# Optimization experiments

Hardware: AMD Instinct MI355X
Metric: run time of the kernel (lower is better)

Reference implementation:

```python
import jax, jax.numpy as jnp
import numpy as np

B, T, C, HS = 4, 2048, 1024, 128

def setup_inputs() -> dict:
    key = jax.random.key(0)
    k0, k1, k2, k3 = jax.random.split(key, 4)
    scale = 1.0 / np.sqrt(C)
    return {
        "x": jax.random.normal(k0, (B, T, C), dtype=jnp.float32),
        "Wk": jax.random.normal(k1, (C, HS), dtype=jnp.float32) * scale,
        "Wq": jax.random.normal(k2, (C, HS), dtype=jnp.float32) * scale,
        "Wv": jax.random.normal(k3, (C, HS), dtype=jnp.float32) * scale,
    }

def reference(x, Wk, Wq, Wv):
    # k, q, v: [B, T, HS]
    k = jnp.einsum('btc,ch->bth', x, Wk)
    q = jnp.einsum('btc,ch->bth', x, Wq)
    v = jnp.einsum('btc,ch->bth', x, Wv)
    hs = k.shape[-1]
    # full T x T scores (no causal mask in source), scaled by head_size**-0.5
    wei = jnp.einsum('bqh,bkh->bqk', q, k) * (hs ** -0.5)
    wei = jax.nn.softmax(wei, axis=-1)
    # dropout p=0.0 -> identity
    out = jnp.einsum('bqk,bkh->bqh', wei, v)
    return out
```

## Files before the change

kernel.cpp:

```cpp
#include <hip/hip_runtime.h>
#include <hip/hip_bf16.h>

typedef float  f32x4 __attribute__((ext_vector_type(4)));
typedef float  f32x8 __attribute__((ext_vector_type(8)));
typedef short  s8v   __attribute__((ext_vector_type(8)));
typedef __bf16 b8v   __attribute__((ext_vector_type(8)));
typedef unsigned int u32;
typedef unsigned short ushort;

#define T_DIM  2048
#define C_DIM  1024


typedef const __attribute__((address_space(1))) u32 gu32;
typedef __attribute__((address_space(3))) u32 lu32;

static __device__ __forceinline__ void glds16(const void* g, void* l) {
  __builtin_amdgcn_global_load_lds((gu32*)g, (lu32*)l, 16, 0, 0);
}

static __device__ __forceinline__ b8v ldb8(const ushort* p) {
  return __builtin_bit_cast(b8v, *reinterpret_cast<const s8v*>(p));
}

static __device__ __forceinline__ b8v cvt8(f32x8 v) {
  b8v r;
#pragma unroll
  for (int i = 0; i < 8; ++i) r[i] = (__bf16)v[i];
  return r;
}

static __device__ __forceinline__ ushort bfu(float f) {
  __bf16 h = (__bf16)f;
  return __builtin_bit_cast(ushort, h);
}

static __device__ __forceinline__ f32x4 mfma16(b8v a, b8v b, f32x4 c) {
  return __builtin_amdgcn_mfma_f32_16x16x32_bf16(a, b, c, 0, 0, 0);
}

#define BAR_VM(N)                                                        \
  asm volatile("s_waitcnt vmcnt(" #N ") lgkmcnt(0)" ::: "memory");       \
  __builtin_amdgcn_s_barrier();                                          \
  asm volatile("" ::: "memory");

#define BAR_PLAIN                                                        \
  asm volatile("" ::: "memory");                                         \
  __builtin_amdgcn_s_barrier();                                          \
  asm volatile("" ::: "memory");

__global__ __launch_bounds__(256) void wconv(const float* __restrict__ Wq,
                                             const float* __restrict__ Wk,
                                             const float* __restrict__ Wv,
                                             ushort* __restrict__ Wt) {
  __shared__ float lds[64][65];
  const int m  = blockIdx.z;
  const int c0 = blockIdx.x * 64;
  const int h0 = blockIdx.y * 64;
  const float* W = (m == 0) ? Wq : (m == 1) ? Wk : Wv;

  const int cl = threadIdx.x >> 4;
  const int h4 = (threadIdx.x & 15) * 4;
#pragma unroll
  for (int i = 0; i < 4; ++i) {
    int c = cl + i * 16;
    float4 v = *reinterpret_cast<const float4*>(W + (c0 + c) * 128 + h0 + h4);
    lds[c][h4] = v.x; lds[c][h4 + 1] = v.y;
    lds[c][h4 + 2] = v.z; lds[c][h4 + 3] = v.w;
  }
  __syncthreads();
  const int hl = threadIdx.x >> 2;
  const int cs = (threadIdx.x & 3) * 16;
  s8v o0, o1;
#pragma unroll
  for (int i = 0; i < 8; ++i) o0[i] = (short)bfu(lds[cs + i][hl]);
#pragma unroll
  for (int i = 0; i < 8; ++i) o1[i] = (short)bfu(lds[cs + 8 + i][hl]);
  ushort* dst = Wt + (m * 128 + h0 + hl) * C_DIM + c0 + cs;
  *reinterpret_cast<s8v*>(dst) = o0;
  *reinterpret_cast<s8v*>(dst + 8) = o1;
}

__global__ __launch_bounds__(256) void proj(const float* __restrict__ x,
                                            const ushort* __restrict__ Wt,
                                            ushort* __restrict__ q,
                                            ushort* __restrict__ k,
                                            ushort* __restrict__ vt) {
  __shared__ __align__(16) ushort Ab[2][32 * 72];
  __shared__ __align__(16) ushort Bb[2][128 * 64];
  __shared__ __align__(16) ushort stage[5120];

  const int t   = threadIdx.x;
  const int w   = t >> 6;
  const int lid = t & 63;
  const int lr  = lid & 15;
  const int g   = lid >> 4;
  const int wr  = w >> 1;
  const int wc  = w & 1;
  const int m   = blockIdx.y;
  const int r0  = blockIdx.x * 32;

  const int arow = t >> 3;
  const int acol = (t & 7) * 8;
  const float* ag = x + (r0 + arow) * C_DIM + acol;

  const int bswz = (((lid & 7) ^ (lid >> 3)) << 4);
  const char* bg = (const char*)(Wt + m * 128 * C_DIM);

  f32x4 acc[4] = {};

#pragma unroll
  for (int j = 0; j < 4; ++j) {
    int h = j * 32 + w * 8 + (lid >> 3);
    glds16(bg + h * 2048 + bswz, (char*)&Bb[0][0] + j * 4096 + w * 1024);
  }
  {
    f32x8 av = *reinterpret_cast<const f32x8*>(ag);
    b8v ac = cvt8(av);
    *reinterpret_cast<s8v*>(&Ab[0][arow * 72 + acol]) =
        __builtin_bit_cast(s8v, ac);
  }
  __syncthreads();

  int cur = 0;
#pragma unroll 1
  for (int i = 0; i < 16; ++i) {
    const int nxt = cur ^ 1;
    f32x8 an;
    if (i < 15) {
      const int kk = (i + 1) * 64;
#pragma unroll
      for (int j = 0; j < 4; ++j) {
        int h = j * 32 + w * 8 + (lid >> 3);
        glds16(bg + h * 2048 + kk * 2 + bswz,
               (char*)&Bb[nxt][0] + j * 4096 + w * 1024);
      }
      an = *reinterpret_cast<const f32x8*>(ag + kk);
    }

#pragma unroll
    for (int kk2 = 0; kk2 < 2; ++kk2) {
      b8v af = ldb8(&Ab[cur][(wr * 16 + lr) * 72 + kk2 * 32 + g * 8]);
#pragma unroll
      for (int cn = 0; cn < 4; ++cn) {
        int h = wc * 64 + cn * 16 + lr;
        int inner = (kk2 * 64 + g * 16) ^ ((h & 7) << 4);
        b8v bf = ldb8(
            (const ushort*)((const char*)&Bb[cur][h * 64] + inner));
        acc[cn] = mfma16(af, bf, acc[cn]);
      }
    }

    if (i < 15) {
      b8v anc = cvt8(an);
      *reinterpret_cast<s8v*>(&Ab[nxt][arow * 72 + acol]) =
          __builtin_bit_cast(s8v, anc);
    }
    __syncthreads();
    cur = nxt;
  }

  if (m < 2) {
#pragma unroll
    for (int cn = 0; cn < 4; ++cn)
#pragma unroll
      for (int j = 0; j < 4; ++j)
        stage[(wr * 16 + 4 * g + j) * 136 + wc * 64 + cn * 16 + lr] =
            bfu(acc[cn][j]);
    __syncthreads();
    ushort* dst = (m == 0) ? q : k;
#pragma unroll
    for (int c = 0; c < 2; ++c) {
      int chunk = c * 256 + t;
      int row = chunk >> 4, col8 = chunk & 15;
      s8v v8 = *reinterpret_cast<const s8v*>(&stage[row * 136 + col8 * 8]);
      *reinterpret_cast<s8v*>(&dst[(r0 + row) * 128 + col8 * 8]) = v8;
    }
  } else {
#pragma unroll
    for (int cn = 0; cn < 4; ++cn)
#pragma unroll
      for (int j = 0; j < 4; ++j)
        stage[(wc * 64 + cn * 16 + lr) * 40 + wr * 16 + 4 * g + j] =
            bfu(acc[cn][j]);
    __syncthreads();
    int b = blockIdx.x >> 6;
    int tbase = (blockIdx.x & 63) * 32;
#pragma unroll
    for (int c = 0; c < 2; ++c) {
      int chunk = c * 256 + t;
      int h = chunk >> 2, t8 = chunk & 3;
      s8v v8 = *reinterpret_cast<const s8v*>(&stage[h * 40 + t8 * 8]);
      *reinterpret_cast<s8v*>(&vt[(b * 128 + h) * T_DIM + tbase + t8 * 8]) = v8;
    }
  }
}

__global__ __launch_bounds__(256) void attn(const ushort* __restrict__ q,
                                            const ushort* __restrict__ k,
                                            const ushort* __restrict__ vt,
                                            float* __restrict__ out) {
  extern __shared__ __align__(16) char smem[];

  const int t   = threadIdx.x;
  const int w   = t >> 6;
  const int lid = t & 63;
  const int lr  = lid & 15;
  const int g   = lid >> 4;
  const int wh  = w >> 1;
  const int wk  = w & 1;
  const int b   = blockIdx.y;
  const int t0  = blockIdx.x * 16;

  const ushort* qp = q + (b * T_DIM + t0) * 128;
  b8v aq[4];
#pragma unroll
  for (int kf = 0; kf < 4; ++kf)
    aq[kf] = ldb8(&qp[lr * 128 + kf * 32 + g * 8]);

  const char* kgb = (const char*)(k + b * T_DIM * 128);
  const char* vgb = (const char*)(vt + b * 128 * T_DIM);
  const char* ksrc[4];
  const char* vsrc[4];
#pragma unroll
  for (int j = 0; j < 4; ++j) {
    ksrc[j] = kgb + (16 * w + 4 * j + (lid >> 4)) * 256 +
              (((lid & 15) ^ (4 * j + (lid >> 4))) << 4);
    vsrc[j] = vgb + ((w * 4 + j) * 8 + (lid >> 3)) * 4096 +
              (((lid & 7) ^ (lid >> 3)) << 4);
  }

  const int rbase = wk * 32 + 8 * (lr >> 2) + (lr & 3);
  int koff[2][4], voff[4];
#pragma unroll
  for (int tt = 0; tt < 2; ++tt)
#pragma unroll
    for (int kf = 0; kf < 4; ++kf)
      koff[tt][kf] = (rbase + 4 * tt) * 256 +
                     (((kf * 4 + g) ^ ((rbase + 4 * tt) & 15)) << 4);
#pragma unroll
  for (int hf = 0; hf < 4; ++hf)
    voff[hf] = 16384 + (wh * 64 + hf * 16 + lr) * 128 +
               (((wk * 4 + g) ^ (lr & 7)) << 4);

  f32x4 of[4] = {};
  float lsum = 0.0f;
  const float scale = 0.08838834764831845f;

#define ATTN_STAGE(KV0, BUF)                                              \
  _Pragma("unroll") for (int j = 0; j < 4; ++j)                           \
      glds16(ksrc[j] + (KV0) * 256,                                       \
             smem + (BUF) * 32768 + (w * 4 + j) * 1024);                  \
  _Pragma("unroll") for (int j = 0; j < 4; ++j)                           \
      glds16(vsrc[j] + (KV0) * 2,                                         \
             smem + (BUF) * 32768 + 16384 + (w * 4 + j) * 1024);

#define ATTN_BODY(BUF)                                                    \
  {                                                                       \
    const char* Kb = smem + (BUF) * 32768;                                \
    b8v kf0[4], kf1[4], vf[4];                                            \
    _Pragma("unroll") for (int kf = 0; kf < 4; ++kf)                      \
        kf0[kf] = ldb8((const ushort*)(Kb + koff[0][kf]));                \
    _Pragma("unroll") for (int kf = 0; kf < 4; ++kf)                      \
        kf1[kf] = ldb8((const ushort*)(Kb + koff[1][kf]));                \
    _Pragma("unroll") for (int hf = 0; hf < 4; ++hf)                      \
        vf[hf] = ldb8((const ushort*)(Kb + voff[hf]));                    \
    f32x4 s0 = {}, s1 = {};                                               \
    __builtin_amdgcn_s_setprio(1);                                        \
    _Pragma("unroll") for (int kf = 0; kf < 4; ++kf) {                    \
      s0 = mfma16(kf0[kf], aq[kf], s0);                                   \
      s1 = mfma16(kf1[kf], aq[kf], s1);                                   \
    }                                                                     \
    __builtin_amdgcn_s_setprio(0);                                        \
    b8v pk;                                                               \
    {                                                                     \
      float p0 = __expf(s0[0] * scale - 4.0f);                            \
      float p1 = __expf(s0[1] * scale - 4.0f);                            \
      float p2 = __expf(s0[2] * scale - 4.0f);                            \
      float p3 = __expf(s0[3] * scale - 4.0f);                            \
      float p4 = __expf(s1[0] * scale - 4.0f);                            \
      float p5 = __expf(s1[1] * scale - 4.0f);                            \
      float p6 = __expf(s1[2] * scale - 4.0f);                            \
      float p7 = __expf(s1[3] * scale - 4.0f);                            \
      lsum += ((p0 + p1) + (p2 + p3)) + ((p4 + p5) + (p6 + p7));          \
      pk[0] = (__bf16)p0; pk[1] = (__bf16)p1;                             \
      pk[2] = (__bf16)p2; pk[3] = (__bf16)p3;                             \
      pk[4] = (__bf16)p4; pk[5] = (__bf16)p5;                             \
      pk[6] = (__bf16)p6; pk[7] = (__bf16)p7;                             \
    }                                                                     \
    __builtin_amdgcn_s_setprio(1);                                        \
    _Pragma("unroll") for (int hf = 0; hf < 4; ++hf)                      \
        of[hf] = mfma16(pk, vf[hf], of[hf]);                              \
    __builtin_amdgcn_s_setprio(0);                                        \
  }

  ATTN_STAGE(0, 0)
  ATTN_STAGE(64, 1)

#pragma unroll 1
  for (int i = 0; i < 31; ++i) {
    BAR_VM(8)
    ATTN_BODY(i & 1)
    BAR_PLAIN
    if (i < 30) { ATTN_STAGE((i + 2) * 64, i & 1) }
  }
  BAR_VM(0)
  ATTN_BODY(1)

#undef ATTN_STAGE
#undef ATTN_BODY

  {
    float r = lsum;
    r += __shfl_xor(r, 16);
    r += __shfl_xor(r, 32);
    lsum = r;
  }

  float* lb = (float*)smem;
  float* ob = (float*)(smem + 256);
  __syncthreads();
  if (wh == 0 && g == 0) lb[wk * 16 + lr] = lsum;
  if (wk == 1) {
#pragma unroll
    for (int hf = 0; hf < 4; ++hf)
#pragma unroll
      for (int j = 0; j < 4; ++j)
        ob[(wh * 16 + 4 * g + j) * 64 + hf * 16 + lr] = of[hf][j];
  }
  __syncthreads();
  if (wk == 0) {
    float inv[4];
#pragma unroll
    for (int j = 0; j < 4; ++j)
      inv[j] = 1.0f / (lb[4 * g + j] + lb[16 + 4 * g + j]);
#pragma unroll
    for (int hf = 0; hf < 4; ++hf)
#pragma unroll
      for (int j = 0; j < 4; ++j) {
        int qrow = 4 * g + j;
        float val = of[hf][j] + ob[(wh * 16 + qrow) * 64 + hf * 16 + lr];
        out[(b * T_DIM + t0 + qrow) * 128 + wh * 64 + hf * 16 + lr] =
            val * inv[j];
      }
  }
}

extern "C" void kernel_launch(void* const* d_in, const int* in_sizes, int n_in,
                              void* d_out, int out_size, void* d_ws,
                              size_t ws_size, hipStream_t stream) {
  const float* x  = (const float*)d_in[0];
  const float* Wk = (const float*)d_in[1];
  const float* Wq = (const float*)d_in[2];
  const float* Wv = (const float*)d_in[3];
  float* out = (float*)d_out;

  char* ws = (char*)d_ws;
  ushort* Wt  = (ushort*)ws;
  ushort* qb  = (ushort*)(ws + (1u << 20));
  ushort* kb  = (ushort*)(ws + 3u * (1u << 20));
  ushort* vtb = (ushort*)(ws + 5u * (1u << 20));

  (void)hipFuncSetAttribute(reinterpret_cast<const void*>(&attn),
                            hipFuncAttributeMaxDynamicSharedMemorySize, 65536);

  wconv<<<dim3(16, 2, 3), dim3(256), 0, stream>>>(Wq, Wk, Wv, Wt);
  proj<<<dim3(256, 3), dim3(256), 0, stream>>>(x, Wt, qb, kb, vtb);
  attn<<<dim3(128, 4), dim3(256), 65536, stream>>>(qb, kb, vtb, out);
}
```

Measured before the change: 56.54 us.

## Use 8-wave attention blocks sharing K/V tiles with a triple-buffered single-barrier pipeline

The attention kernel now runs 512 threads per block covering 32 query rows, two groups of four waves, so each staged K/V tile in LDS serves twice as many queries and per-thread global-to-LDS loads are halved. The double-buffered loop with two barriers per iteration becomes a three-buffer ring with one barrier per iteration, issuing the next stage before computing the current one. This cuts redundant K/V fetches and barrier stalls but uses 96KB of LDS per block and halves the grid, which may reduce occupancy.

Result: faster. 51.62 us (-8.7%).

```diff
diff --git a/kernel.cpp b/kernel.cpp
--- a/kernel.cpp
+++ b/kernel.cpp
@@ -41,11 +41,6 @@
 
 #define BAR_VM(N)                                                        \
   asm volatile("s_waitcnt vmcnt(" #N ") lgkmcnt(0)" ::: "memory");       \
-  __builtin_amdgcn_s_barrier();                                          \
-  asm volatile("" ::: "memory");
-
-#define BAR_PLAIN                                                        \
-  asm volatile("" ::: "memory");                                         \
   __builtin_amdgcn_s_barrier();                                          \
   asm volatile("" ::: "memory");
 
@@ -196,7 +191,7 @@
   }
 }
 
-__global__ __launch_bounds__(256) void attn(const ushort* __restrict__ q,
+__global__ __launch_bounds__(512) void attn(const ushort* __restrict__ q,
                                             const ushort* __restrict__ k,
                                             const ushort* __restrict__ vt,
                                             float* __restrict__ out) {
@@ -207,12 +202,13 @@
   const int lid = t & 63;
   const int lr  = lid & 15;
   const int g   = lid >> 4;
-  const int wh  = w >> 1;
+  const int wq  = w >> 2;
+  const int wh  = (w >> 1) & 1;
   const int wk  = w & 1;
   const int b   = blockIdx.y;
-  const int t0  = blockIdx.x * 16;
-
-  const ushort* qp = q + (b * T_DIM + t0) * 128;
+  const int t0  = blockIdx.x * 32;
+
+  const ushort* qp = q + (b * T_DIM + t0 + wq * 16) * 128;
   b8v aq[4];
 #pragma unroll
   for (int kf = 0; kf < 4; ++kf)
@@ -220,13 +216,13 @@
 
   const char* kgb = (const char*)(k + b * T_DIM * 128);
   const char* vgb = (const char*)(vt + b * 128 * T_DIM);
-  const char* ksrc[4];
-  const char* vsrc[4];
-#pragma unroll
-  for (int j = 0; j < 4; ++j) {
-    ksrc[j] = kgb + (16 * w + 4 * j + (lid >> 4)) * 256 +
-              (((lid & 15) ^ (4 * j + (lid >> 4))) << 4);
-    vsrc[j] = vgb + ((w * 4 + j) * 8 + (lid >> 3)) * 4096 +
+  const char* ksrc[2];
+  const char* vsrc[2];
+#pragma unroll
+  for (int j = 0; j < 2; ++j) {
+    int krow = 8 * w + 4 * j + (lid >> 4);
+    ksrc[j] = kgb + krow * 256 + (((lid & 15) ^ (krow & 15)) << 4);
+    vsrc[j] = vgb + ((w * 2 + j) * 8 + (lid >> 3)) * 4096 +
               (((lid & 7) ^ (lid >> 3)) << 4);
   }
 
@@ -248,12 +244,12 @@
   const float scale = 0.08838834764831845f;
 
 #define ATTN_STAGE(KV0, BUF)                                              \
-  _Pragma("unroll") for (int j = 0; j < 4; ++j)                           \
+  _Pragma("unroll") for (int j = 0; j < 2; ++j)                           \
       glds16(ksrc[j] + (KV0) * 256,                                       \
-             smem + (BUF) * 32768 + (w * 4 + j) * 1024);                  \
-  _Pragma("unroll") for (int j = 0; j < 4; ++j)                           \
+             smem + (BUF) * 32768 + (w * 2 + j) * 1024);                  \
+  _Pragma("unroll") for (int j = 0; j < 2; ++j)                           \
       glds16(vsrc[j] + (KV0) * 2,                                         \
-             smem + (BUF) * 32768 + 16384 + (w * 4 + j) * 1024);
+             smem + (BUF) * 32768 + 16384 + (w * 2 + j) * 1024);
 
 #define ATTN_BODY(BUF)                                                    \
   {                                                                       \
@@ -297,15 +293,19 @@
   ATTN_STAGE(0, 0)
   ATTN_STAGE(64, 1)
 
+  int cur = 0;
 #pragma unroll 1
   for (int i = 0; i < 31; ++i) {
-    BAR_VM(8)
-    ATTN_BODY(i & 1)
-    BAR_PLAIN
-    if (i < 30) { ATTN_STAGE((i + 2) * 64, i & 1) }
+    BAR_VM(4)
+    if (i < 30) {
+      int nb = cur + 2; if (nb >= 3) nb -= 3;
+      ATTN_STAGE((i + 2) * 64, nb)
+    }
+    ATTN_BODY(cur)
+    ++cur; if (cur == 3) cur = 0;
   }
   BAR_VM(0)
-  ATTN_BODY(1)
+  ATTN_BODY(cur)
 
 #undef ATTN_STAGE
 #undef ATTN_BODY
@@ -320,27 +320,29 @@
   float* lb = (float*)smem;
   float* ob = (float*)(smem + 256);
   __syncthreads();
-  if (wh == 0 && g == 0) lb[wk * 16 + lr] = lsum;
+  if (wh == 0 && g == 0) lb[(wk * 2 + wq) * 16 + lr] = lsum;
   if (wk == 1) {
 #pragma unroll
     for (int hf = 0; hf < 4; ++hf)
 #pragma unroll
       for (int j = 0; j < 4; ++j)
-        ob[(wh * 16 + 4 * g + j) * 64 + hf * 16 + lr] = of[hf][j];
+        ob[((wq * 2 + wh) * 16 + 4 * g + j) * 64 + hf * 16 + lr] = of[hf][j];
   }
   __syncthreads();
   if (wk == 0) {
     float inv[4];
 #pragma unroll
     for (int j = 0; j < 4; ++j)
-      inv[j] = 1.0f / (lb[4 * g + j] + lb[16 + 4 * g + j]);
+      inv[j] = 1.0f / (lb[(0 * 2 + wq) * 16 + 4 * g + j] +
+                       lb[(1 * 2 + wq) * 16 + 4 * g + j]);
 #pragma unroll
     for (int hf = 0; hf < 4; ++hf)
 #pragma unroll
       for (int j = 0; j < 4; ++j) {
         int qrow = 4 * g + j;
-        float val = of[hf][j] + ob[(wh * 16 + qrow) * 64 + hf * 16 + lr];
-        out[(b * T_DIM + t0 + qrow) * 128 + wh * 64 + hf * 16 + lr] =
+        float val = of[hf][j] +
+                    ob[((wq * 2 + wh) * 16 + qrow) * 64 + hf * 16 + lr];
+        out[(b * T_DIM + t0 + wq * 16 + qrow) * 128 + wh * 64 + hf * 16 + lr] =
             val * inv[j];
       }
   }
@@ -362,9 +364,9 @@
   ushort* vtb = (ushort*)(ws + 5u * (1u << 20));
 
   (void)hipFuncSetAttribute(reinterpret_cast<const void*>(&attn),
-                            hipFuncAttributeMaxDynamicSharedMemorySize, 65536);
+                            hipFuncAttributeMaxDynamicSharedMemorySize, 98304);
 
   wconv<<<dim3(16, 2, 3), dim3(256), 0, stream>>>(Wq, Wk, Wv, Wt);
   proj<<<dim3(256, 3), dim3(256), 0, stream>>>(x, Wt, qb, kb, vtb);
-  attn<<<dim3(128, 4), dim3(256), 65536, stream>>>(qb, kb, vtb, out);
-}
+  attn<<<dim3(64, 4), dim3(512), 98304, stream>>>(qb, kb, vtb, out);
+}
```
